# Optimization experiments

Hardware: AMD Instinct MI355X
Metric: run time of the kernel (lower is better)

## Reference

```python
import jax, jax.numpy as jnp
import numpy as np

DIM = 256
HEADS = 8
WS = 8            # window size
SHIFT = 4
MLP_HID = 1024
EPS = 1e-5
HEAD_DIM = DIM // HEADS
SCALE = HEAD_DIM ** -0.5
N = WS * WS       # tokens per window


def _rel_pos_index():
    coords = np.stack(np.meshgrid(np.arange(WS), np.arange(WS), indexing='ij'))  # [2,ws,ws]
    flat = coords.reshape(2, -1)                                                  # [2,N]
    rel = flat[:, :, None] - flat[:, None, :]                                     # [2,N,N]
    rel = rel.transpose(1, 2, 0)                                                  # [N,N,2]
    rel[:, :, 0] += WS - 1
    rel[:, :, 1] += WS - 1
    rel[:, :, 0] *= 2 * WS - 1
    return jnp.asarray(rel.sum(-1))                                               # [N,N] int

REL_IDX = _rel_pos_index()


def layernorm(x, g, b):
    mu = x.mean(-1, keepdims=True)
    var = ((x - mu) ** 2).mean(-1, keepdims=True)
    return (x - mu) * jax.lax.rsqrt(var + EPS) * g + b


def setup_inputs() -> dict:
    key = jax.random.key(0)
    ks = jax.random.split(key, 16)
    s = 0.02
    return {
        'x': jax.random.normal(ks[0], (16, 16384, DIM), jnp.float32),
        'qkv_w': jax.random.normal(ks[1], (DIM, 3 * DIM), jnp.float32) * s,
        'qkv_b': jnp.zeros((3 * DIM,), jnp.float32),
        'proj_w': jax.random.normal(ks[2], (DIM, DIM), jnp.float32) * s,
        'proj_b': jnp.zeros((DIM,), jnp.float32),
        'rpb_table': jax.random.normal(ks[3], ((2 * WS - 1) ** 2, HEADS), jnp.float32) * s,
        'ln1_g': jnp.ones((DIM,), jnp.float32),
        'ln1_b': jnp.zeros((DIM,), jnp.float32),
        'ln2_g': jnp.ones((DIM,), jnp.float32),
        'ln2_b': jnp.zeros((DIM,), jnp.float32),
        'mlp_w1': jax.random.normal(ks[4], (DIM, MLP_HID), jnp.float32) * s,
        'mlp_b1': jnp.zeros((MLP_HID,), jnp.float32),
        'mlp_w2': jax.random.normal(ks[5], (MLP_HID, DIM), jnp.float32) * s,
        'mlp_b2': jnp.zeros((DIM,), jnp.float32),
        'H': 128,
        'W': 128,
    }


def reference(x, qkv_w, qkv_b, proj_w, proj_b, rpb_table,
              ln1_g, ln1_b, ln2_g, ln2_b, mlp_w1, mlp_b1, mlp_w2, mlp_b2, H, W):
    B, L, C = x.shape
    shortcut = x

    h = layernorm(x, ln1_g, ln1_b).reshape(B, H, W, C)
    if SHIFT > 0:
        h = jnp.roll(h, (-SHIFT, -SHIFT), axis=(1, 2))

    # window partition: [B,H,W,C] -> [B*nW, N, C]
    h = h.reshape(B, H // WS, WS, W // WS, WS, C).transpose(0, 1, 3, 2, 4, 5)
    xw = h.reshape(-1, N, C)
    Bw = xw.shape[0]

    # window attention
    qkv = (xw @ qkv_w + qkv_b).reshape(Bw, N, 3, HEADS, HEAD_DIM)
    q, k, v = qkv[:, :, 0], qkv[:, :, 1], qkv[:, :, 2]        # [Bw,N,H,D]
    attn = jnp.einsum('bnhd,bmhd->bhnm', q, k) * SCALE         # [Bw,H,N,N]
    bias = rpb_table[REL_IDX.reshape(-1)].reshape(N, N, HEADS).transpose(2, 0, 1)
    attn = jax.nn.softmax(attn + bias[None], axis=-1)
    out = jnp.einsum('bhnm,bmhd->bnhd', attn, v).reshape(Bw, N, C)
    out = out @ proj_w + proj_b

    # window reverse
    out = out.reshape(B, H // WS, W // WS, WS, WS, C).transpose(0, 1, 3, 2, 4, 5).reshape(B, H, W, C)
    if SHIFT > 0:
        out = jnp.roll(out, (SHIFT, SHIFT), axis=(1, 2))
    out = out.reshape(B, L, C)

    h2 = layernorm(out, ln2_g, ln2_b)
    mlp = jax.nn.gelu(h2 @ mlp_w1 + mlp_b1, approximate=False) @ mlp_w2 + mlp_b2
    return shortcut + out + mlp
```

## Files before the change

### kernel.cpp

```cpp
#include <hip/hip_runtime.h>
#include <math.h>

typedef short bfrag __attribute__((ext_vector_type(8)));
typedef float ffrag __attribute__((ext_vector_type(4)));

#define MFMA16(a, b, c) __builtin_amdgcn_mfma_f32_16x16x32_bf16((a), (b), (c), 0, 0, 0)

__device__ __align__(16) unsigned short g_wt[786432];

__device__ __forceinline__ unsigned bf16b(float f) {
  unsigned u = __float_as_uint(f);
  return (u + 0x7FFFu + ((u >> 16) & 1u)) >> 16;
}
__device__ __forceinline__ unsigned pk2(float lo, float hi) {
  return bf16b(lo) | (bf16b(hi) << 16);
}
__device__ __forceinline__ float bf2f(unsigned u) {
  return __uint_as_float(u << 16);
}
__device__ __forceinline__ float gelu_f(float u) {
  const float z = 1.5957691216057308f * (u + 0.044715f * u * u * u);
  return u * __builtin_amdgcn_rcpf(1.f + __expf(-z));
}

__global__ void conv_w(const float* __restrict__ qkv_w, const float* __restrict__ proj_w,
                       const float* __restrict__ w1, const float* __restrict__ w2) {
  const int idx = blockIdx.x * 256 + threadIdx.x;
  const float* src; int c, k2, C, K, ofs;
  if (idx < 98304)       { src = qkv_w;  C = 768;  K = 256;  c = idx % 768;  k2 = idx / 768;  ofs = 0; }
  else if (idx < 131072) { int i = idx - 98304;  src = proj_w; C = 256;  K = 256;  c = i % 256;  k2 = i / 256;  ofs = 196608; }
  else if (idx < 262144) { int i = idx - 131072; src = w1;     C = 1024; K = 256;  c = i % 1024; k2 = i / 1024; ofs = 262144; }
  else                   { int i = idx - 262144; src = w2;     C = 256;  K = 1024; c = i % 256;  k2 = i / 256;  ofs = 524288; }
  const float lo = src[(2 * k2) * C + c];
  const float hi = src[(2 * k2 + 1) * C + c];
  *(unsigned*)&g_wt[ofs + c * K + 2 * k2] = pk2(lo, hi);
}

__device__ __forceinline__ int swz(int row, int col, int C) {
  return row * (C * 2) + ((((col >> 3) ^ (row & 7)) << 4) + ((col & 7) << 1));
}
__device__ __forceinline__ bfrag ldfrag(const char* lds, int outer, int k0, int C) {
  const int l = threadIdx.x & 63;
  return *(const bfrag*)(lds + swz(outer + (l & 15), k0 + ((l >> 4) << 3), C));
}

__device__ __forceinline__ void stage128(char* lds, const unsigned short* __restrict__ src,
                                         long rowBase, int strideShorts, int kOfs) {
  const int wv = threadIdx.x >> 6, l = threadIdx.x & 63;
  #pragma unroll
  for (int p = 0; p < 4; ++p) {
    const int base = wv * 1024 + p * 8192;
    const int off = base + l * 16;
    const int row = off >> 8;
    const int ss = ((off & 255) >> 4) ^ (row & 7);
    const unsigned short* g = src + (rowBase + row) * (long)strideShorts + kOfs + ss * 8;
    __builtin_amdgcn_global_load_lds((const __attribute__((address_space(1))) void*)g,
                                     (__attribute__((address_space(3))) void*)(lds + base),
                                     16, 0, 0);
  }
}

template <int DSTROWB>
__device__ __forceinline__ void glds_stage(char* lds, const unsigned short* src,
                                           int srcRowShorts, int bytes) {
  const int wv = threadIdx.x >> 6, l = threadIdx.x & 63;
  for (int base = wv * 1024; base < bytes; base += 8192) {
    const int off = base + l * 16;
    const int row = off / DSTROWB;
    const int slot = (off % DSTROWB) >> 4;
    const int ss = slot ^ (row & 7);
    const unsigned short* g = src + row * srcRowShorts + ss * 8;
    __builtin_amdgcn_global_load_lds((const __attribute__((address_space(1))) void*)g,
                                     (__attribute__((address_space(3))) void*)(lds + base),
                                     16, 0, 0);
  }
}

__device__ __forceinline__ void mm_core128(const char* AX, const char* BW, ffrag acc[2][4]) {
  const int wv = threadIdx.x >> 6;
  const int rh = wv >> 2, cq = wv & 3;
  #pragma unroll
  for (int ks = 0; ks < 4; ++ks) {
    const bfrag aw0 = ldfrag(BW, cq * 32, ks * 32, 128);
    const bfrag aw1 = ldfrag(BW, cq * 32 + 16, ks * 32, 128);
    #pragma unroll
    for (int nt = 0; nt < 4; ++nt) {
      const bfrag xb = ldfrag(AX, rh * 64 + nt * 16, ks * 32, 128);
      acc[0][nt] = MFMA16(aw0, xb, acc[0][nt]);
      acc[1][nt] = MFMA16(aw1, xb, acc[1][nt]);
    }
  }
}

__device__ __forceinline__ void ln_pack(float d0, float d1, float d2, float d3,
                                        const float* g, const float* bb, int lane,
                                        unsigned& o0, unsigned& o1) {
  float s = d0 + d1 + d2 + d3;
  #pragma unroll
  for (int o = 32; o; o >>= 1) s += __shfl_xor(s, o);
  const float mu = s * (1.f / 256.f);
  d0 -= mu; d1 -= mu; d2 -= mu; d3 -= mu;
  float q = d0 * d0 + d1 * d1 + d2 * d2 + d3 * d3;
  #pragma unroll
  for (int o = 32; o; o >>= 1) q += __shfl_xor(q, o);
  const float vv = q * (1.f / 256.f) + 1e-5f;
  float rs = rsqrtf(vv);
  rs = rs * (1.5f - 0.5f * vv * rs * rs);
  const float4 g4 = *(const float4*)(g + lane * 4);
  const float4 b4 = *(const float4*)(bb + lane * 4);
  o0 = pk2(d0 * rs * g4.x + b4.x, d1 * rs * g4.y + b4.y);
  o1 = pk2(d2 * rs * g4.z + b4.z, d3 * rs * g4.w + b4.w);
}

__global__ __launch_bounds__(512) void ln1_k(const float* __restrict__ x,
    const float* __restrict__ g, const float* __restrict__ bb,
    unsigned short* __restrict__ XB, long rowOfs) {
  const int wv = threadIdx.x >> 6, l = threadIdx.x & 63;
  const long lrow = (long)blockIdx.x * 8 + wv;
  const float4 v = *(const float4*)(x + (rowOfs + lrow) * 256 + l * 4);
  unsigned o0, o1;
  ln_pack(v.x, v.y, v.z, v.w, g, bb, l, o0, o1);
  unsigned short* dp = XB + lrow * 256 + l * 4;
  *(unsigned*)dp = o0; *(unsigned*)(dp + 2) = o1;
}

__global__ __launch_bounds__(512, 4) void gemm_qkv(const unsigned short* __restrict__ XB,
    const float* __restrict__ qkv_b, unsigned short* __restrict__ QKV) {
  __shared__ __align__(16) char smem[65536];
  char* AX = smem; char* BW = smem + 32768;
  const int mb = blockIdx.x, nb = blockIdx.y;
  ffrag acc[2][4];
  #pragma unroll
  for (int a = 0; a < 2; ++a)
    #pragma unroll
    for (int n = 0; n < 4; ++n) { ffrag z = {0.f, 0.f, 0.f, 0.f}; acc[a][n] = z; }
  #pragma unroll
  for (int kc = 0; kc < 2; ++kc) {
    stage128(AX, XB, (long)mb * 128, 256, kc * 128);
    stage128(BW, g_wt, (long)nb * 128, 256, kc * 128);
    __syncthreads();
    mm_core128(AX, BW, acc);
    __syncthreads();
  }
  const int l = threadIdx.x & 63, wv = threadIdx.x >> 6;
  const int rh = wv >> 2, cq = wv & 3;
  const float sc = (nb < 2) ? 0.17677669529663687f : 1.f;
  #pragma unroll
  for (int mt = 0; mt < 2; ++mt) {
    const int cg = nb * 128 + cq * 32 + mt * 16 + ((l >> 4) << 2);
    const float4 bq = *(const float4*)(qkv_b + cg);
    #pragma unroll
    for (int nt = 0; nt < 4; ++nt) {
      const long row = (long)mb * 128 + rh * 64 + nt * 16 + (l & 15);
      unsigned short* dp = QKV + row * 768 + cg;
      *(unsigned*)dp       = pk2((acc[mt][nt][0] + bq.x) * sc, (acc[mt][nt][1] + bq.y) * sc);
      *(unsigned*)(dp + 2) = pk2((acc[mt][nt][2] + bq.z) * sc, (acc[mt][nt][3] + bq.w) * sc);
    }
  }
}

__global__ __launch_bounds__(512, 4) void gemm_proj(const unsigned short* __restrict__ O,
    const float* __restrict__ proj_b, unsigned short* __restrict__ outw) {
  __shared__ __align__(16) char smem[65536];
  char* AX = smem; char* BW = smem + 32768;
  const int mb = blockIdx.x, nb = blockIdx.y;
  ffrag acc[2][4];
  #pragma unroll
  for (int a = 0; a < 2; ++a)
    #pragma unroll
    for (int n = 0; n < 4; ++n) { ffrag z = {0.f, 0.f, 0.f, 0.f}; acc[a][n] = z; }
  #pragma unroll
  for (int kc = 0; kc < 2; ++kc) {
    stage128(AX, O, (long)mb * 128, 256, kc * 128);
    stage128(BW, g_wt + 196608, (long)nb * 128, 256, kc * 128);
    __syncthreads();
    mm_core128(AX, BW, acc);
    __syncthreads();
  }
  const int l = threadIdx.x & 63, wv = threadIdx.x >> 6;
  const int rh = wv >> 2, cq = wv & 3;
  #pragma unroll
  for (int mt = 0; mt < 2; ++mt) {
    const int cg = nb * 128 + cq * 32 + mt * 16 + ((l >> 4) << 2);
    const float4 pb = *(const float4*)(proj_b + cg);
    #pragma unroll
    for (int nt = 0; nt < 4; ++nt) {
      const long row = (long)mb * 128 + rh * 64 + nt * 16 + (l & 15);
      unsigned short* dp = outw + row * 256 + cg;
      *(unsigned*)dp       = pk2(acc[mt][nt][0] + pb.x, acc[mt][nt][1] + pb.y);
      *(unsigned*)(dp + 2) = pk2(acc[mt][nt][2] + pb.z, acc[mt][nt][3] + pb.w);
    }
  }
}

__global__ __launch_bounds__(512, 4) void attn_core(const unsigned short* __restrict__ QKV,
    const float* __restrict__ rpb, unsigned short* __restrict__ O, int bofs) {
  __shared__ __align__(16) char smem[81920];
  char* KL = smem;
  char* VT = smem + 32768;
  char* PB = smem + 65536;
  const int t = threadIdx.x, wv = t >> 6, l = t & 63;
  const int blk = blockIdx.x;
  const int b = blk >> 8, w = blk & 255;
  const int wi = w >> 4, wj = w & 15;
  const int bi0 = wi * 8 + 4, bj0 = wj * 8 + 4;
  const ffrag ZERO4 = {0.f, 0.f, 0.f, 0.f};

  #define SROW(r) (((long)b << 14) + (((bi0 + ((r) >> 3)) & 127) << 7) + ((bj0 + ((r) & 7)) & 127))
  #define GROW(r) (((long)(bofs + b) << 14) + (((bi0 + ((r) >> 3)) & 127) << 7) + ((bj0 + ((r) & 7)) & 127))

  #pragma unroll
  for (int p = 0; p < 4; ++p) {
    const int base = wv * 1024 + p * 8192;
    const int off = base + l * 16;
    const int kv = off >> 9;
    const int ss = ((off & 511) >> 4) ^ (kv & 7);
    const unsigned short* g = QKV + SROW(kv) * 768 + 256 + ss * 8;
    __builtin_amdgcn_global_load_lds((const __attribute__((address_space(1))) void*)g,
                                     (__attribute__((address_space(3))) void*)(KL + base),
                                     16, 0, 0);
  }

  {
    const int rp = t & 31, dh = t >> 5;
    const unsigned short* v0p = QKV + SROW(2 * rp) * 768 + 512 + dh * 16;
    const unsigned short* v1p = QKV + SROW(2 * rp + 1) * 768 + 512 + dh * 16;
    const bfrag a0 = *(const bfrag*)v0p, a1 = *(const bfrag*)(v0p + 8);
    const bfrag c0 = *(const bfrag*)v1p, c1 = *(const bfrag*)(v1p + 8);
    #pragma unroll
    for (int j = 0; j < 8; ++j) {
      const unsigned w0 = ((unsigned)(unsigned short)a0[j]) | (((unsigned)(unsigned short)c0[j]) << 16);
      const unsigned w1 = ((unsigned)(unsigned short)a1[j]) | (((unsigned)(unsigned short)c1[j]) << 16);
      *(unsigned*)(VT + swz(dh * 16 + j, 2 * rp, 64)) = w0;
      *(unsigned*)(VT + swz(dh * 16 + 8 + j, 2 * rp, 64)) = w1;
    }
  }
  __syncthreads();

  const int qt = wv & 3, hh = wv >> 2;
  char* myPB = PB + wv * 2048;
  const int colb = l & 15;
  const int rbase = qt * 16 + ((l >> 4) << 2);

  for (int i = 0; i < 4; ++i) {
    const int h = 2 * i + hh;
    const int hk = h * 32;
    const int qr = qt * 16 + (l & 15);
    const bfrag aq = *(const bfrag*)(QKV + SROW(qr) * 768 + hk + ((l >> 4) << 3));
    ffrag s[4];
    #pragma unroll
    for (int nt = 0; nt < 4; ++nt) {
      const bfrag bk = ldfrag(KL, nt * 16, hk, 256);
      s[nt] = MFMA16(aq, bk, ZERO4);
    }
    float pr[4][4], mx[4], sm[4];
    #pragma unroll
    for (int reg = 0; reg < 4; ++reg) mx[reg] = -3e38f;
    #pragma unroll
    for (int nt = 0; nt < 4; ++nt)
      #pragma unroll
      for (int reg = 0; reg < 4; ++reg) {
        const int rr = rbase + reg, cc = nt * 16 + colb;
        const int idx = ((rr >> 3) - (cc >> 3) + 7) * 15 + ((rr & 7) - (cc & 7) + 7);
        pr[nt][reg] = s[nt][reg] + rpb[idx * 8 + h];
        mx[reg] = fmaxf(mx[reg], pr[nt][reg]);
      }
    #pragma unroll
    for (int reg = 0; reg < 4; ++reg) {
      #pragma unroll
      for (int o = 1; o < 16; o <<= 1) mx[reg] = fmaxf(mx[reg], __shfl_xor(mx[reg], o));
      sm[reg] = 0.f;
    }
    #pragma unroll
    for (int nt = 0; nt < 4; ++nt)
      #pragma unroll
      for (int reg = 0; reg < 4; ++reg) {
        pr[nt][reg] = __expf(pr[nt][reg] - mx[reg]);
        sm[reg] += pr[nt][reg];
      }
    #pragma unroll
    for (int reg = 0; reg < 4; ++reg) {
      #pragma unroll
      for (int o = 1; o < 16; o <<= 1) sm[reg] += __shfl_xor(sm[reg], o);
      sm[reg] = 1.f / sm[reg];
    }
    #pragma unroll
    for (int nt = 0; nt < 4; ++nt)
      #pragma unroll
      for (int reg = 0; reg < 4; ++reg)
        *(unsigned short*)(myPB + swz(((l >> 4) << 2) + reg, nt * 16 + colb, 64)) =
            (unsigned short)bf16b(pr[nt][reg] * sm[reg]);

    ffrag o0 = ZERO4, o1 = ZERO4;
    #pragma unroll
    for (int ks = 0; ks < 2; ++ks) {
      const bfrag ap = ldfrag(myPB, 0, ks * 32, 64);
      const bfrag bv0 = ldfrag(VT, hk, ks * 32, 64);
      const bfrag bv1 = ldfrag(VT, hk + 16, ks * 32, 64);
      o0 = MFMA16(ap, bv0, o0);
      o1 = MFMA16(ap, bv1, o1);
    }
    #pragma unroll
    for (int reg = 0; reg < 4; ++reg) {
      const long orow = GROW(rbase + reg);
      O[orow * 256 + hk + colb] = (unsigned short)bf16b(o0[reg]);
      O[orow * 256 + hk + 16 + colb] = (unsigned short)bf16b(o1[reg]);
    }
  }
  #undef SROW
  #undef GROW
}

__global__ __launch_bounds__(512, 4) void swin_mlp(
    const float* __restrict__ x, const unsigned short* __restrict__ outw,
    const float* __restrict__ ln2g, const float* __restrict__ ln2b,
    const float* __restrict__ b1, const float* __restrict__ b2,
    float* __restrict__ y)
{
  __shared__ __align__(16) char smem[73728];
  char* H2 = smem;
  char* WS = smem + 32768;
  char* HD = smem + 65536;
  const int t = threadIdx.x, wv = t >> 6, l = t & 63;
  const long base = (long)blockIdx.x << 6;

  #pragma unroll
  for (int i = 0; i < 8; ++i) {
    const int r = wv * 8 + i;
    const uint2 raw = *(const uint2*)(outw + (base + r) * 256 + l * 4);
    unsigned o0, o1;
    ln_pack(bf2f(raw.x & 0xFFFFu), bf2f(raw.x >> 16), bf2f(raw.y & 0xFFFFu), bf2f(raw.y >> 16),
            ln2g, ln2b, l, o0, o1);
    *(unsigned*)(H2 + swz(r, l * 4, 256)) = o0;
    *(unsigned*)(H2 + swz(r, l * 4 + 2, 256)) = o1;
  }
  __syncthreads();

  const int mq = wv >> 1, nq = (wv & 1) << 1;

  ffrag acc2[2][4];
  #pragma unroll
  for (int mt = 0; mt < 2; ++mt)
    #pragma unroll
    for (int nt = 0; nt < 4; ++nt) { ffrag z = {0.f, 0.f, 0.f, 0.f}; acc2[mt][nt] = z; }

  for (int ch = 0; ch < 16; ++ch) {
    glds_stage<512>(WS, g_wt + 262144 + ch * 64 * 256, 256, 32768);
    __syncthreads();
    ffrag a1[2];
    { ffrag z = {0.f, 0.f, 0.f, 0.f}; a1[0] = z; a1[1] = z; }
    #pragma unroll
    for (int ks = 0; ks < 8; ++ks) {
      const bfrag a = ldfrag(WS, mq * 16, ks * 32, 256);
      const bfrag bb0 = ldfrag(H2, nq * 16, ks * 32, 256);
      const bfrag bb1 = ldfrag(H2, (nq + 1) * 16, ks * 32, 256);
      a1[0] = MFMA16(a, bb0, a1[0]);
      a1[1] = MFMA16(a, bb1, a1[1]);
    }
    __syncthreads();

    const int c0 = mq * 16 + ((l >> 4) << 2);
    const float4 b14 = *(const float4*)(b1 + ch * 64 + c0);
    #pragma unroll
    for (int nt = 0; nt < 2; ++nt) {
      const int rr = (nq + nt) * 16 + (l & 15);
      const float g0 = gelu_f(a1[nt][0] + b14.x);
      const float g1 = gelu_f(a1[nt][1] + b14.y);
      const float g2 = gelu_f(a1[nt][2] + b14.z);
      const float g3 = gelu_f(a1[nt][3] + b14.w);
      *(unsigned*)(HD + swz(rr, c0, 64)) = pk2(g0, g1);
      *(unsigned*)(HD + swz(rr, c0 + 2, 64)) = pk2(g2, g3);
    }
    glds_stage<128>(WS, g_wt + 524288 + ch * 64, 1024, 32768);
    __syncthreads();

    #pragma unroll
    for (int ks = 0; ks < 2; ++ks) {
      const bfrag am0 = ldfrag(WS, (wv * 2) * 16, ks * 32, 64);
      const bfrag am1 = ldfrag(WS, (wv * 2 + 1) * 16, ks * 32, 64);
      #pragma unroll
      for (int nt = 0; nt < 4; ++nt) {
        const bfrag bb = ldfrag(HD, nt * 16, ks * 32, 64);
        acc2[0][nt] = MFMA16(am0, bb, acc2[0][nt]);
        acc2[1][nt] = MFMA16(am1, bb, acc2[1][nt]);
      }
    }
    __syncthreads();
  }

  #pragma unroll
  for (int mt = 0; mt < 2; ++mt) {
    const int c0 = (wv * 2 + mt) * 16 + ((l >> 4) << 2);
    const float4 b24 = *(const float4*)(b2 + c0);
    #pragma unroll
    for (int nt = 0; nt < 4; ++nt) {
      const long row = base + nt * 16 + (l & 15);
      const float4 xv = *(const float4*)(x + row * 256 + c0);
      const uint2 ov = *(const uint2*)(outw + row * 256 + c0);
      float4 res;
      res.x = acc2[mt][nt][0] + b24.x + xv.x + bf2f(ov.x & 0xFFFFu);
      res.y = acc2[mt][nt][1] + b24.y + xv.y + bf2f(ov.x >> 16);
      res.z = acc2[mt][nt][2] + b24.z + xv.z + bf2f(ov.y & 0xFFFFu);
      res.w = acc2[mt][nt][3] + b24.w + xv.w + bf2f(ov.y >> 16);
      *(float4*)(y + row * 256 + c0) = res;
    }
  }
}

extern "C" void kernel_launch(void* const* d_in, const int* in_sizes, int n_in,
                              void* d_out, int out_size, void* d_ws, size_t ws_size,
                              hipStream_t stream) {
  (void)in_sizes; (void)n_in; (void)out_size; (void)ws_size;
  const float* x      = (const float*)d_in[0];
  const float* qkv_w  = (const float*)d_in[1];
  const float* qkv_b  = (const float*)d_in[2];
  const float* proj_w = (const float*)d_in[3];
  const float* proj_b = (const float*)d_in[4];
  const float* rpb    = (const float*)d_in[5];
  const float* ln1g   = (const float*)d_in[6];
  const float* ln1b   = (const float*)d_in[7];
  const float* ln2g   = (const float*)d_in[8];
  const float* ln2b   = (const float*)d_in[9];
  const float* w1     = (const float*)d_in[10];
  const float* b1     = (const float*)d_in[11];
  const float* w2     = (const float*)d_in[12];
  const float* b2     = (const float*)d_in[13];
  float* y = (float*)d_out;
  char* ws = (char*)d_ws;

  unsigned short* XB   = (unsigned short*)(ws);
  unsigned short* QKV  = (unsigned short*)(ws + 33554432);
  unsigned short* Obuf = (unsigned short*)(ws + 134217728);
  unsigned short* outw = (unsigned short*)(ws);

  hipLaunchKernelGGL(conv_w, dim3(1536), dim3(256), 0, stream, qkv_w, proj_w, w1, w2);
  for (int g = 0; g < 4; ++g) {
    hipLaunchKernelGGL(ln1_k, dim3(8192), dim3(512), 0, stream,
                       x, ln1g, ln1b, XB, (long)g * 65536);
    hipLaunchKernelGGL(gemm_qkv, dim3(512, 6), dim3(512), 0, stream, XB, qkv_b, QKV);
    hipLaunchKernelGGL(attn_core, dim3(1024), dim3(512), 0, stream, QKV, rpb, Obuf, g * 4);
  }
  hipLaunchKernelGGL(gemm_proj, dim3(2048, 2), dim3(512), 0, stream, Obuf, proj_b, outw);
  hipLaunchKernelGGL(swin_mlp, dim3(4096), dim3(512), 0, stream,
                     x, outw, ln2g, ln2b, b1, b2, y);
}
```

Measured before the change: 1.197 ms.

## Double-buffer MLP weight tiles to overlap global-to-LDS loads with MFMA

```diff
diff --git a/kernel.cpp b/kernel.cpp
--- a/kernel.cpp
+++ b/kernel.cpp
@@ -311,18 +311,26 @@
   #undef GROW
 }
 
-__global__ __launch_bounds__(512, 4) void swin_mlp(
+__global__ __launch_bounds__(512, 2) void swin_mlp(
     const float* __restrict__ x, const unsigned short* __restrict__ outw,
     const float* __restrict__ ln2g, const float* __restrict__ ln2b,
     const float* __restrict__ b1, const float* __restrict__ b2,
     float* __restrict__ y)
 {
-  __shared__ __align__(16) char smem[73728];
-  char* H2 = smem;
-  char* WS = smem + 32768;
-  char* HD = smem + 65536;
+  __shared__ __align__(16) char smem[106496];
+  char* H2  = smem;
+  char* WSa = smem + 32768;
+  char* WSb = smem + 65536;
+  char* HD  = smem + 98304;
   const int t = threadIdx.x, wv = t >> 6, l = t & 63;
   const long base = (long)blockIdx.x << 6;
+
+  const int mq = wv >> 1, nq = (wv & 1) << 1;
+  const int c0 = mq * 16 + ((l >> 4) << 2);
+
+  glds_stage<512>(WSa, g_wt + 262144, 256, 32768);
+  float4 b14 = *(const float4*)(b1 + c0);
+  glds_stage<128>(WSb, g_wt + 524288, 1024, 32768);
 
   #pragma unroll
   for (int i = 0; i < 8; ++i) {
@@ -336,8 +344,6 @@
   }
   __syncthreads();
 
-  const int mq = wv >> 1, nq = (wv & 1) << 1;
-
   ffrag acc2[2][4];
   #pragma unroll
   for (int mt = 0; mt < 2; ++mt)
@@ -345,22 +351,16 @@
     for (int nt = 0; nt < 4; ++nt) { ffrag z = {0.f, 0.f, 0.f, 0.f}; acc2[mt][nt] = z; }
 
   for (int ch = 0; ch < 16; ++ch) {
-    glds_stage<512>(WS, g_wt + 262144 + ch * 64 * 256, 256, 32768);
-    __syncthreads();
     ffrag a1[2];
     { ffrag z = {0.f, 0.f, 0.f, 0.f}; a1[0] = z; a1[1] = z; }
     #pragma unroll
     for (int ks = 0; ks < 8; ++ks) {
-      const bfrag a = ldfrag(WS, mq * 16, ks * 32, 256);
+      const bfrag a = ldfrag(WSa, mq * 16, ks * 32, 256);
       const bfrag bb0 = ldfrag(H2, nq * 16, ks * 32, 256);
       const bfrag bb1 = ldfrag(H2, (nq + 1) * 16, ks * 32, 256);
       a1[0] = MFMA16(a, bb0, a1[0]);
       a1[1] = MFMA16(a, bb1, a1[1]);
     }
-    __syncthreads();
-
-    const int c0 = mq * 16 + ((l >> 4) << 2);
-    const float4 b14 = *(const float4*)(b1 + ch * 64 + c0);
     #pragma unroll
     for (int nt = 0; nt < 2; ++nt) {
       const int rr = (nq + nt) * 16 + (l & 15);
@@ -371,13 +371,15 @@
       *(unsigned*)(HD + swz(rr, c0, 64)) = pk2(g0, g1);
       *(unsigned*)(HD + swz(rr, c0 + 2, 64)) = pk2(g2, g3);
     }
-    glds_stage<128>(WS, g_wt + 524288 + ch * 64, 1024, 32768);
-    __syncthreads();
+    asm volatile("s_waitcnt vmcnt(0) lgkmcnt(0)" ::: "memory");
+    __builtin_amdgcn_s_barrier();
+    asm volatile("" ::: "memory");
+    if (ch < 15) glds_stage<512>(WSa, g_wt + 262144 + (ch + 1) * 64 * 256, 256, 32768);
 
     #pragma unroll
     for (int ks = 0; ks < 2; ++ks) {
-      const bfrag am0 = ldfrag(WS, (wv * 2) * 16, ks * 32, 64);
-      const bfrag am1 = ldfrag(WS, (wv * 2 + 1) * 16, ks * 32, 64);
+      const bfrag am0 = ldfrag(WSb, (wv * 2) * 16, ks * 32, 64);
+      const bfrag am1 = ldfrag(WSb, (wv * 2 + 1) * 16, ks * 32, 64);
       #pragma unroll
       for (int nt = 0; nt < 4; ++nt) {
         const bfrag bb = ldfrag(HD, nt * 16, ks * 32, 64);
@@ -385,24 +387,30 @@
         acc2[1][nt] = MFMA16(am1, bb, acc2[1][nt]);
       }
     }
-    __syncthreads();
+    asm volatile("s_waitcnt vmcnt(0) lgkmcnt(0)" ::: "memory");
+    __builtin_amdgcn_s_barrier();
+    asm volatile("" ::: "memory");
+    if (ch < 15) {
+      b14 = *(const float4*)(b1 + (ch + 1) * 64 + c0);
+      glds_stage<128>(WSb, g_wt + 524288 + (ch + 1) * 64, 1024, 32768);
+    }
   }
 
   #pragma unroll
   for (int mt = 0; mt < 2; ++mt) {
-    const int c0 = (wv * 2 + mt) * 16 + ((l >> 4) << 2);
-    const float4 b24 = *(const float4*)(b2 + c0);
+    const int cc0 = (wv * 2 + mt) * 16 + ((l >> 4) << 2);
+    const float4 b24 = *(const float4*)(b2 + cc0);
     #pragma unroll
     for (int nt = 0; nt < 4; ++nt) {
       const long row = base + nt * 16 + (l & 15);
-      const float4 xv = *(const float4*)(x + row * 256 + c0);
-      const uint2 ov = *(const uint2*)(outw + row * 256 + c0);
+      const float4 xv = *(const float4*)(x + row * 256 + cc0);
+      const uint2 ov = *(const uint2*)(outw + row * 256 + cc0);
       float4 res;
       res.x = acc2[mt][nt][0] + b24.x + xv.x + bf2f(ov.x & 0xFFFFu);
       res.y = acc2[mt][nt][1] + b24.y + xv.y + bf2f(ov.x >> 16);
       res.z = acc2[mt][nt][2] + b24.z + xv.z + bf2f(ov.y & 0xFFFFu);
       res.w = acc2[mt][nt][3] + b24.w + xv.w + bf2f(ov.y >> 16);
-      *(float4*)(y + row * 256 + c0) = res;
+      *(float4*)(y + row * 256 + cc0) = res;
     }
   }
 }
```

Measured after the change: 1.273 ms. 6.3% more time.
